# Optimization experiments

Measured on AMD Instinct MI355X. Metric: run time of the kernel, lower is better.

## Reference

```python
import jax, jax.numpy as jnp
import numpy as np

N_NODES = 100000
N_EDGES = 1600000
N_FEAT = 128
HIDDEN = 64
NUM_GRAPHS = 64


def setup_inputs() -> dict:
    key = jax.random.key(0)
    ks = jax.random.split(key, 10)
    x = jax.random.normal(ks[0], (N_NODES, N_FEAT), dtype=jnp.float32)
    W = jax.random.normal(ks[1], (N_FEAT, HIDDEN), dtype=jnp.float32) * (1.0 / np.sqrt(N_FEAT))
    b = jax.random.normal(ks[2], (HIDDEN,), dtype=jnp.float32) * 0.01
    W1 = jax.random.normal(ks[3], (HIDDEN, 16), dtype=jnp.float32) * (1.0 / np.sqrt(HIDDEN))
    b1 = jax.random.normal(ks[4], (16,), dtype=jnp.float32) * 0.01
    W2 = jax.random.normal(ks[5], (16, 1), dtype=jnp.float32) * 0.25
    b2 = jax.random.normal(ks[6], (1,), dtype=jnp.float32) * 0.01
    edge_index = jax.random.randint(ks[7], (2, N_EDGES), 0, N_NODES, dtype=jnp.int64)
    batch = jnp.sort(jax.random.randint(ks[8], (N_NODES,), 0, NUM_GRAPHS, dtype=jnp.int64))
    return {"x": x, "W": W, "b": b, "W1": W1, "b1": b1, "W2": W2, "b2": b2,
            "edge_index": edge_index, "batch": batch, "num_graphs": NUM_GRAPHS}


def reference(x, W, b, W1, b1, W2, b2, edge_index, batch, num_graphs):
    N = x.shape[0]
    # GCNConv: h = D^-1/2 (A + I) D^-1/2 (x W) + b
    h = x @ W  # [N, H]
    loops = jnp.arange(N, dtype=edge_index.dtype)
    src = jnp.concatenate([edge_index[0], loops])  # source nodes (with self-loops)
    dst = jnp.concatenate([edge_index[1], loops])  # target nodes
    deg = jax.ops.segment_sum(jnp.ones(dst.shape, h.dtype), dst, num_segments=N)
    dis = jnp.where(deg > 0, jax.lax.rsqrt(deg), 0.0)  # deg^-1/2, 0 for isolated
    norm = dis[src] * dis[dst]  # [E+N]
    msg = h[src] * norm[:, None]  # gather + normalize
    agg = jax.ops.segment_sum(msg, dst, num_segments=N) + b  # scatter-add + bias
    hn = jax.nn.relu(agg)
    # global_add_pool over graphs
    u = jax.ops.segment_sum(hn, batch, num_segments=num_graphs)  # [G, H]
    out = jax.nn.relu(u @ W1 + b1) @ W2 + b2  # [G, 1]
    return out.reshape(-1)
```

## Files before the change

kernel.cpp:

```cpp
#include <hip/hip_runtime.h>

#define N_NODES   100000
#define N_FEAT    128
#define N_EDGES   1600000
#define HIDDEN    64
#define NUM_GRAPHS 64
#define CHUNK   8192
#define NCHUNK  ((N_EDGES + CHUNK - 1) / CHUNK)
#define BSHIFT  8
#define NBUCKET ((N_NODES + 255) >> 8)
#define OFFS_W  (NBUCKET + 1)
#define CAP     4800
#define WT_BLOCKS 4
#define GEMM_GRID ((N_NODES + 127) / 128)

typedef unsigned int  uint32;
typedef unsigned short ushort16;

typedef __attribute__((ext_vector_type(8))) __bf16 bf16x8;
typedef __attribute__((ext_vector_type(4))) float  f32x4;
union Frag8 { bf16x8 v; unsigned short s[8]; uint4 q; };

static __device__ __forceinline__ unsigned short f2bf(float f) {
    uint32 u = __float_as_uint(f);
    u += 0x7fffu + ((u >> 16) & 1u);
    return (unsigned short)(u >> 16);
}

__global__ __launch_bounds__(512) void k_pre(const float* __restrict__ W,
                                             ushort16* __restrict__ Wt,
                                             const int* __restrict__ ei,
                                             int* __restrict__ src_out,
                                             unsigned char* __restrict__ dst8,
                                             int* __restrict__ offs) {
    __shared__ int hist[512];
    __shared__ int excl[512];
    __shared__ int ssrc[CHUNK];
    __shared__ int sdst[CHUNK];

    if (blockIdx.x < WT_BLOCKS) {
        const int base = blockIdx.x * 2048 + threadIdx.x;
#pragma unroll
        for (int j = 0; j < 4; ++j) {
            const int idx = base + j * 512;
            const int k = idx >> 6, n = idx & 63;
            Wt[n * N_FEAT + k] = f2bf(W[idx]);
        }
        return;
    }

    const int c = blockIdx.x - WT_BLOCKS;
    const int base = c * CHUNK;
    const int n = min(CHUNK, N_EDGES - base);
    const int t = threadIdx.x;
    hist[t] = 0;
    __syncthreads();

    int es[CHUNK / 512], ed[CHUNK / 512], rk[CHUNK / 512];
#pragma unroll
    for (int k = 0; k < CHUNK / 512; ++k) {
        const int i = t + k * 512;
        if (i < n) {
            ed[k] = __builtin_nontemporal_load(&ei[N_EDGES + base + i]);
            es[k] = __builtin_nontemporal_load(&ei[base + i]);
            rk[k] = atomicAdd(&hist[ed[k] >> BSHIFT], 1);
        }
    }
    __syncthreads();

    const int cnt = hist[t];
    for (int off = 1; off < 512; off <<= 1) {
        const int v = (t >= off) ? hist[t - off] : 0;
        __syncthreads();
        hist[t] += v;
        __syncthreads();
    }
    excl[t] = hist[t] - cnt;
    __syncthreads();
    if (t <= NBUCKET) offs[c * OFFS_W + t] = base + excl[t];

#pragma unroll
    for (int k = 0; k < CHUNK / 512; ++k) {
        const int i = t + k * 512;
        if (i < n) {
            const int pos = excl[ed[k] >> BSHIFT] + rk[k];
            ssrc[pos] = es[k];
            sdst[pos] = ed[k];
        }
    }
    __syncthreads();

    for (int i = t; i < n; i += 512)
        src_out[base + i] = ssrc[i];
    for (int i = t * 4; i < n; i += 2048) {
        const uint32 p = (uint32)(sdst[i] & 255)
                       | ((uint32)(sdst[i + 1] & 255) << 8)
                       | ((uint32)(sdst[i + 2] & 255) << 16)
                       | ((uint32)(sdst[i + 3] & 255) << 24);
        *(uint32*)&dst8[base + i] = p;
    }
}

__global__ __launch_bounds__(512) void k_mid(const float* __restrict__ x,
                                             const ushort16* __restrict__ Wt,
                                             ushort16* __restrict__ hb,
                                             const int* __restrict__ offs,
                                             const int* __restrict__ src_tmp,
                                             const unsigned char* __restrict__ dst8,
                                             int* __restrict__ srcs,
                                             int* __restrict__ row_ptr,
                                             int* __restrict__ row_end,
                                             float* __restrict__ dis) {
    __shared__ int hist[256];
    __shared__ int nxt[256];
    __shared__ int segb[NCHUNK];
    __shared__ int pre[NCHUNK + 1];
    __shared__ int sc[256];
    __shared__ int ssrc[CAP];
    __shared__ int sb;

    if (blockIdx.x >= NBUCKET) {
        const int t    = threadIdx.x;
        const int lane = t & 63;
        const int wv   = t >> 6;
        const int m15  = lane & 15;
        const int quad = lane >> 4;
        const int base = (blockIdx.x - NBUCKET) * 128 + wv * 16;
        const int arow = min(base + m15, N_NODES - 1);

        const float* xr = &x[(size_t)arow * N_FEAT + quad * 8];
        float4 xa[4][2];
#pragma unroll
        for (int kc = 0; kc < 4; ++kc) {
            xa[kc][0] = *(const float4*)&xr[kc * 32];
            xa[kc][1] = *(const float4*)&xr[kc * 32 + 4];
        }

        Frag8 bf[4][4];
#pragma unroll
        for (int nt = 0; nt < 4; ++nt) {
            const ushort16* wr = &Wt[(nt * 16 + m15) * N_FEAT + quad * 8];
#pragma unroll
            for (int kc = 0; kc < 4; ++kc)
                bf[nt][kc].q = *(const uint4*)&wr[kc * 32];
        }

        Frag8 af[4];
#pragma unroll
        for (int kc = 0; kc < 4; ++kc) {
            const float* f = (const float*)&xa[kc][0];
#pragma unroll
            for (int j = 0; j < 8; ++j) af[kc].s[j] = f2bf(f[j]);
        }

        f32x4 acc[4];
#pragma unroll
        for (int nt = 0; nt < 4; ++nt) acc[nt] = (f32x4){0.f, 0.f, 0.f, 0.f};

#pragma unroll
        for (int kc = 0; kc < 4; ++kc)
#pragma unroll
            for (int nt = 0; nt < 4; ++nt)
                acc[nt] = __builtin_amdgcn_mfma_f32_16x16x32_bf16(af[kc].v, bf[nt][kc].v,
                                                                  acc[nt], 0, 0, 0);

#pragma unroll
        for (int r = 0; r < 4; ++r) {
            const int orow = base + quad * 4 + r;
            if (orow < N_NODES) {
#pragma unroll
                for (int nt = 0; nt < 4; ++nt)
                    hb[(size_t)orow * HIDDEN + nt * 16 + m15] = f2bf(acc[nt][r]);
            }
        }
        return;
    }

    const int b = blockIdx.x;
    const int lo = b << BSHIFT;
    const int t = threadIdx.x;

    if (t < 256) hist[t] = 0;
    if (t == 0) sb = 0;
    __syncthreads();

    int len = 0;
    if (t < NCHUNK) {
        const int s0 = offs[t * OFFS_W + b];
        const int s1 = offs[t * OFFS_W + b + 1];
        segb[t] = s0;
        len = s1 - s0;
        atomicAdd(&sb, s0 - t * CHUNK);
    }
    if (t < 256) sc[t] = (t < NCHUNK) ? len : 0;
    __syncthreads();
    for (int off = 1; off < 256; off <<= 1) {
        int v = 0;
        if (t < 256 && t >= off) v = sc[t - off];
        __syncthreads();
        if (t < 256) sc[t] += v;
        __syncthreads();
    }
    if (t == 0) pre[0] = 0;
    if (t < NCHUNK) pre[t + 1] = sc[t];
    __syncthreads();

    const int total  = pre[NCHUNK];
    const int bstart = sb;
    const bool fits  = (total <= CAP);

    int es[(CAP + 511) / 512], ed[(CAP + 511) / 512], rk[(CAP + 511) / 512];
    int ne = 0;
    if (fits) {
        for (int e = t; e < total; e += 512) {
            int l2 = 0, h2 = NCHUNK;
            while (h2 - l2 > 1) { const int mid = (l2 + h2) >> 1;
                                  if (pre[mid] <= e) l2 = mid; else h2 = mid; }
            const int gidx = segb[l2] + (e - pre[l2]);
            const int d = dst8[gidx];
            const int s = src_tmp[gidx];
            es[ne] = s; ed[ne] = d;
            rk[ne] = atomicAdd(&hist[d], 1);
            ++ne;
        }
    } else {
        const int lane = t & 63, wv = t >> 6;
        for (int c = wv; c < NCHUNK; c += 8)
            for (int i = segb[c] + lane; i < segb[c] + (pre[c + 1] - pre[c]); i += 64)
                atomicAdd(&hist[dst8[i]], 1);
    }
    __syncthreads();

    const int cnt = (t < 256) ? hist[t] : 0;
    for (int off = 1; off < 256; off <<= 1) {
        int v = 0;
        if (t < 256 && t >= off) v = hist[t - off];
        __syncthreads();
        if (t < 256) hist[t] += v;
        __syncthreads();
    }
    if (t < 256) {
        const int excl = hist[t] - cnt;
        nxt[t] = excl;
        const int node = lo + t;
        if (node < N_NODES) {
            row_ptr[node] = bstart + excl;
            row_end[node] = bstart + excl + cnt;
            dis[node]     = rsqrtf((float)cnt + 1.0f);
        }
    }
    __syncthreads();

    if (fits) {
        for (int k = 0; k < ne; ++k)
            ssrc[nxt[ed[k]] + rk[k]] = es[k];
        __syncthreads();
        for (int i = t; i < total; i += 512)
            srcs[bstart + i] = ssrc[i];
    } else {
        const int lane = t & 63, wv = t >> 6;
        for (int c = wv; c < NCHUNK; c += 8)
            for (int i = segb[c] + lane; i < segb[c] + (pre[c + 1] - pre[c]); i += 64) {
                const int d = dst8[i];
                const int pos = atomicAdd(&nxt[d], 1);
                srcs[bstart + pos] = src_tmp[i];
            }
    }
}

__global__ __launch_bounds__(256) void agg_kernel(const int* __restrict__ row_ptr,
                                                  const int* __restrict__ row_end,
                                                  const int* __restrict__ srcs,
                                                  const ushort16* __restrict__ hb,
                                                  const float* __restrict__ dis,
                                                  const float* __restrict__ bias,
                                                  const int* __restrict__ batch,
                                                  float* __restrict__ u) {
    __shared__ float sp[32][HIDDEN + 1];
    __shared__ int gbs[32];
    const int t = threadIdx.x;
    const int lane = t & 63;
    const int wv = t >> 6;
    const int g = lane >> 3;
    const int k = lane & 7;
    const int kb = lane & 56;
    const int base = blockIdx.x * 32;
    const int node = base + wv * 8 + g;
    const int beg = row_ptr[node];
    const int end = row_end[node];
    const int deg = end - beg;
    const float dn = dis[node];

    int dmax = deg;
    dmax = max(dmax, __shfl_xor(dmax, 8));
    dmax = max(dmax, __shfl_xor(dmax, 16));
    dmax = max(dmax, __shfl_xor(dmax, 32));

    float acc[8];
#pragma unroll
    for (int j = 0; j < 8; ++j) acc[j] = 0.f;

    for (int i0 = 0; i0 < dmax; i0 += 8) {
        int idx = beg + i0 + k;
        idx = min(idx, end - 1);
        idx = max(idx, 0);
        const int s8 = srcs[idx];
        const float w8 = dis[s8] * dn;

        int   si[8];
        float wi[8];
#pragma unroll
        for (int j = 0; j < 8; ++j) {
            si[j] = __shfl(s8, kb | j);
            const float w = __shfl(w8, kb | j);
            wi[j] = (i0 + j < deg) ? w : 0.f;
        }
        uint4 v[8];
#pragma unroll
        for (int j = 0; j < 8; ++j)
            v[j] = *(const uint4*)&hb[(size_t)si[j] * HIDDEN + k * 8];
#pragma unroll
        for (int j = 0; j < 8; ++j) {
            acc[0] = fmaf(__uint_as_float(v[j].x << 16),         wi[j], acc[0]);
            acc[1] = fmaf(__uint_as_float(v[j].x & 0xffff0000u), wi[j], acc[1]);
            acc[2] = fmaf(__uint_as_float(v[j].y << 16),         wi[j], acc[2]);
            acc[3] = fmaf(__uint_as_float(v[j].y & 0xffff0000u), wi[j], acc[3]);
            acc[4] = fmaf(__uint_as_float(v[j].z << 16),         wi[j], acc[4]);
            acc[5] = fmaf(__uint_as_float(v[j].z & 0xffff0000u), wi[j], acc[5]);
            acc[6] = fmaf(__uint_as_float(v[j].w << 16),         wi[j], acc[6]);
            acc[7] = fmaf(__uint_as_float(v[j].w & 0xffff0000u), wi[j], acc[7]);
        }
    }

    {
        const uint4 hv = *(const uint4*)&hb[(size_t)node * HIDDEN + k * 8];
        const float d2 = dn * dn;
        const float4 b0 = *(const float4*)&bias[k * 8];
        const float4 b1 = *(const float4*)&bias[k * 8 + 4];
        float4 r0, r1;
        r0.x = fmaxf(fmaf(__uint_as_float(hv.x << 16),         d2, acc[0]) + b0.x, 0.f);
        r0.y = fmaxf(fmaf(__uint_as_float(hv.x & 0xffff0000u), d2, acc[1]) + b0.y, 0.f);
        r0.z = fmaxf(fmaf(__uint_as_float(hv.y << 16),         d2, acc[2]) + b0.z, 0.f);
        r0.w = fmaxf(fmaf(__uint_as_float(hv.y & 0xffff0000u), d2, acc[3]) + b0.w, 0.f);
        r1.x = fmaxf(fmaf(__uint_as_float(hv.z << 16),         d2, acc[4]) + b1.x, 0.f);
        r1.y = fmaxf(fmaf(__uint_as_float(hv.z & 0xffff0000u), d2, acc[5]) + b1.y, 0.f);
        r1.z = fmaxf(fmaf(__uint_as_float(hv.w << 16),         d2, acc[6]) + b1.z, 0.f);
        r1.w = fmaxf(fmaf(__uint_as_float(hv.w & 0xffff0000u), d2, acc[7]) + b1.w, 0.f);
        *(float4*)&sp[wv * 8 + g][k * 8]     = r0;
        *(float4*)&sp[wv * 8 + g][k * 8 + 4] = r1;
    }
    if (t < 32) gbs[t] = batch[base + t];
    __syncthreads();

    if (t < 64) {
        float a = sp[0][t];
        int cg = gbs[0];
        for (int r = 1; r < 32; ++r) {
            const int gr = gbs[r];
            const float vv = sp[r][t];
            if (gr == cg) a += vv;
            else { atomicAdd(&u[cg * HIDDEN + t], a); cg = gr; a = vv; }
        }
        atomicAdd(&u[cg * HIDDEN + t], a);
    }
}

__global__ __launch_bounds__(64) void mlp_kernel(const float* __restrict__ u,
                                                 const float* __restrict__ W1,
                                                 const float* __restrict__ b1,
                                                 const float* __restrict__ W2,
                                                 const float* __restrict__ b2,
                                                 float* __restrict__ out) {
    __shared__ float W1s[HIDDEN * 16];
    __shared__ float W2s[16];
    __shared__ float b1s[16];
    const int t = threadIdx.x;
    for (int i = t; i < HIDDEN * 16; i += 64) W1s[i] = W1[i];
    if (t < 16) { W2s[t] = W2[t]; b1s[t] = b1[t]; }
    __syncthreads();
    if (t < NUM_GRAPHS) {
        float uu[HIDDEN];
#pragma unroll
        for (int k = 0; k < HIDDEN; ++k) uu[k] = u[t * HIDDEN + k];
        float o = b2[0];
#pragma unroll
        for (int j = 0; j < 16; ++j) {
            float s = b1s[j];
#pragma unroll
            for (int k = 0; k < HIDDEN; ++k) s = fmaf(uu[k], W1s[k * 16 + j], s);
            o = fmaf(fmaxf(s, 0.f), W2s[j], o);
        }
        out[t] = o;
    }
}

extern "C" void kernel_launch(void* const* d_in, const int* in_sizes, int n_in,
                              void* d_out, int out_size, void* d_ws, size_t ws_size,
                              hipStream_t stream) {
    const float* x  = (const float*)d_in[0];
    const float* W  = (const float*)d_in[1];
    const float* b  = (const float*)d_in[2];
    const float* W1 = (const float*)d_in[3];
    const float* b1 = (const float*)d_in[4];
    const float* W2 = (const float*)d_in[5];
    const float* b2 = (const float*)d_in[6];
    const int*   ei = (const int*)d_in[7];
    const int* batch = (const int*)d_in[8];
    float* out = (float*)d_out;

    ushort16* hb       = (ushort16*)d_ws;
    int*      src_tmp  = (int*)(hb + (size_t)N_NODES * HIDDEN);
    unsigned char* dst8 = (unsigned char*)(src_tmp + N_EDGES);
    int*      srcs     = (int*)(dst8 + N_EDGES);
    int*      offs     = srcs + N_EDGES;
    int*      row_ptr  = offs + NCHUNK * OFFS_W;
    int*      row_end  = row_ptr + N_NODES;
    float*    dis      = (float*)(row_end + N_NODES);
    float*    u        = dis + N_NODES;
    ushort16* Wtg      = (ushort16*)(u + NUM_GRAPHS * HIDDEN);

    hipMemsetAsync(u, 0, NUM_GRAPHS * HIDDEN * sizeof(float), stream);

    k_pre<<<WT_BLOCKS + NCHUNK, 512, 0, stream>>>(W, Wtg, ei, src_tmp, dst8, offs);
    k_mid<<<NBUCKET + GEMM_GRID, 512, 0, stream>>>(x, Wtg, hb, offs, src_tmp, dst8,
                                                   srcs, row_ptr, row_end, dis);
    agg_kernel<<<N_NODES / 32, 256, 0, stream>>>(row_ptr, row_end, srcs, hb, dis, b, batch, u);
    mlp_kernel<<<1, 64, 0, stream>>>(u, W1, b1, W2, b2, out);
}
```

Measured before the change: 177.4 us.

## Prescale features by source degree norm and prefetch neighbor indices in aggregation

A new k_scale kernel multiplies each row of the bf16 hidden features by dis[node] once, so the aggregation loop no longer gathers dis[src] per edge and the destination normalization is applied once at the end. The aggregation loop now iterates per-node degree instead of the group maximum and software-prefetches the next batch of source indices. It also halves CHUNK (more chunks, a 512-wide scan) to give the bucketing pass more parallel blocks. The extra kernel adds a full read-write pass over hb and a second bf16 rounding of the scaled values, and per-lane divergent loop trip counts may add divergence.

Measured after the change: 175.4 us. No clear change (-1.1%).

```diff
diff --git a/kernel.cpp b/kernel.cpp
--- a/kernel.cpp
+++ b/kernel.cpp
@@ -5,7 +5,7 @@
 #define N_EDGES   1600000
 #define HIDDEN    64
 #define NUM_GRAPHS 64
-#define CHUNK   8192
+#define CHUNK   4096
 #define NCHUNK  ((N_EDGES + CHUNK - 1) / CHUNK)
 #define BSHIFT  8
 #define NBUCKET ((N_NODES + 255) >> 8)
@@ -115,7 +115,7 @@
     __shared__ int nxt[256];
     __shared__ int segb[NCHUNK];
     __shared__ int pre[NCHUNK + 1];
-    __shared__ int sc[256];
+    __shared__ int sc[512];
     __shared__ int ssrc[CAP];
     __shared__ int sb;
 
@@ -192,13 +192,12 @@
         len = s1 - s0;
         atomicAdd(&sb, s0 - t * CHUNK);
     }
-    if (t < 256) sc[t] = (t < NCHUNK) ? len : 0;
-    __syncthreads();
-    for (int off = 1; off < 256; off <<= 1) {
-        int v = 0;
-        if (t < 256 && t >= off) v = sc[t - off];
-        __syncthreads();
-        if (t < 256) sc[t] += v;
+    sc[t] = len;
+    __syncthreads();
+    for (int off = 1; off < 512; off <<= 1) {
+        const int v = (t >= off) ? sc[t - off] : 0;
+        __syncthreads();
+        sc[t] += v;
         __syncthreads();
     }
     if (t == 0) pre[0] = 0;
@@ -266,6 +265,23 @@
                 srcs[bstart + pos] = src_tmp[i];
             }
     }
+}
+
+__global__ __launch_bounds__(256) void k_scale(ushort16* __restrict__ hb,
+                                               const float* __restrict__ dis) {
+    const int i = blockIdx.x * 256 + threadIdx.x;
+    const float dn = dis[i >> 3];
+    uint4 v = *(const uint4*)&hb[(size_t)i * 8];
+    uint4 r;
+    r.x = (uint32)f2bf(__uint_as_float(v.x << 16) * dn)
+        | ((uint32)f2bf(__uint_as_float(v.x & 0xffff0000u) * dn) << 16);
+    r.y = (uint32)f2bf(__uint_as_float(v.y << 16) * dn)
+        | ((uint32)f2bf(__uint_as_float(v.y & 0xffff0000u) * dn) << 16);
+    r.z = (uint32)f2bf(__uint_as_float(v.z << 16) * dn)
+        | ((uint32)f2bf(__uint_as_float(v.z & 0xffff0000u) * dn) << 16);
+    r.w = (uint32)f2bf(__uint_as_float(v.w << 16) * dn)
+        | ((uint32)f2bf(__uint_as_float(v.w & 0xffff0000u) * dn) << 16);
+    *(uint4*)&hb[(size_t)i * 8] = r;
 }
 
 __global__ __launch_bounds__(256) void agg_kernel(const int* __restrict__ row_ptr,
@@ -291,61 +307,53 @@
     const int deg = end - beg;
     const float dn = dis[node];
 
-    int dmax = deg;
-    dmax = max(dmax, __shfl_xor(dmax, 8));
-    dmax = max(dmax, __shfl_xor(dmax, 16));
-    dmax = max(dmax, __shfl_xor(dmax, 32));
-
     float acc[8];
 #pragma unroll
     for (int j = 0; j < 8; ++j) acc[j] = 0.f;
 
-    for (int i0 = 0; i0 < dmax; i0 += 8) {
-        int idx = beg + i0 + k;
-        idx = min(idx, end - 1);
-        idx = max(idx, 0);
-        const int s8 = srcs[idx];
-        const float w8 = dis[s8] * dn;
-
-        int   si[8];
-        float wi[8];
-#pragma unroll
-        for (int j = 0; j < 8; ++j) {
-            si[j] = __shfl(s8, kb | j);
-            const float w = __shfl(w8, kb | j);
-            wi[j] = (i0 + j < deg) ? w : 0.f;
-        }
+    int pidx = max(min(beg + k, end - 1), 0);
+    int s8 = srcs[pidx];
+
+    for (int i0 = 0; i0 < deg; i0 += 8) {
+        const int rem = deg - i0;
+        const int cur = s8;
+        if (i0 + 8 < deg)
+            s8 = srcs[min(beg + i0 + 8 + k, end - 1)];
+
+        int si[8];
+#pragma unroll
+        for (int j = 0; j < 8; ++j) si[j] = __shfl(cur, kb | j);
         uint4 v[8];
 #pragma unroll
         for (int j = 0; j < 8; ++j)
             v[j] = *(const uint4*)&hb[(size_t)si[j] * HIDDEN + k * 8];
 #pragma unroll
         for (int j = 0; j < 8; ++j) {
-            acc[0] = fmaf(__uint_as_float(v[j].x << 16),         wi[j], acc[0]);
-            acc[1] = fmaf(__uint_as_float(v[j].x & 0xffff0000u), wi[j], acc[1]);
-            acc[2] = fmaf(__uint_as_float(v[j].y << 16),         wi[j], acc[2]);
-            acc[3] = fmaf(__uint_as_float(v[j].y & 0xffff0000u), wi[j], acc[3]);
-            acc[4] = fmaf(__uint_as_float(v[j].z << 16),         wi[j], acc[4]);
-            acc[5] = fmaf(__uint_as_float(v[j].z & 0xffff0000u), wi[j], acc[5]);
-            acc[6] = fmaf(__uint_as_float(v[j].w << 16),         wi[j], acc[6]);
-            acc[7] = fmaf(__uint_as_float(v[j].w & 0xffff0000u), wi[j], acc[7]);
+            const float m = (j < rem) ? 1.f : 0.f;
+            acc[0] = fmaf(__uint_as_float(v[j].x << 16),         m, acc[0]);
+            acc[1] = fmaf(__uint_as_float(v[j].x & 0xffff0000u), m, acc[1]);
+            acc[2] = fmaf(__uint_as_float(v[j].y << 16),         m, acc[2]);
+            acc[3] = fmaf(__uint_as_float(v[j].y & 0xffff0000u), m, acc[3]);
+            acc[4] = fmaf(__uint_as_float(v[j].z << 16),         m, acc[4]);
+            acc[5] = fmaf(__uint_as_float(v[j].z & 0xffff0000u), m, acc[5]);
+            acc[6] = fmaf(__uint_as_float(v[j].w << 16),         m, acc[6]);
+            acc[7] = fmaf(__uint_as_float(v[j].w & 0xffff0000u), m, acc[7]);
         }
     }
 
     {
         const uint4 hv = *(const uint4*)&hb[(size_t)node * HIDDEN + k * 8];
-        const float d2 = dn * dn;
         const float4 b0 = *(const float4*)&bias[k * 8];
         const float4 b1 = *(const float4*)&bias[k * 8 + 4];
         float4 r0, r1;
-        r0.x = fmaxf(fmaf(__uint_as_float(hv.x << 16),         d2, acc[0]) + b0.x, 0.f);
-        r0.y = fmaxf(fmaf(__uint_as_float(hv.x & 0xffff0000u), d2, acc[1]) + b0.y, 0.f);
-        r0.z = fmaxf(fmaf(__uint_as_float(hv.y << 16),         d2, acc[2]) + b0.z, 0.f);
-        r0.w = fmaxf(fmaf(__uint_as_float(hv.y & 0xffff0000u), d2, acc[3]) + b0.w, 0.f);
-        r1.x = fmaxf(fmaf(__uint_as_float(hv.z << 16),         d2, acc[4]) + b1.x, 0.f);
-        r1.y = fmaxf(fmaf(__uint_as_float(hv.z & 0xffff0000u), d2, acc[5]) + b1.y, 0.f);
-        r1.z = fmaxf(fmaf(__uint_as_float(hv.w << 16),         d2, acc[6]) + b1.z, 0.f);
-        r1.w = fmaxf(fmaf(__uint_as_float(hv.w & 0xffff0000u), d2, acc[7]) + b1.w, 0.f);
+        r0.x = fmaxf(fmaf(acc[0] + __uint_as_float(hv.x << 16),         dn, b0.x), 0.f);
+        r0.y = fmaxf(fmaf(acc[1] + __uint_as_float(hv.x & 0xffff0000u), dn, b0.y), 0.f);
+        r0.z = fmaxf(fmaf(acc[2] + __uint_as_float(hv.y << 16),         dn, b0.z), 0.f);
+        r0.w = fmaxf(fmaf(acc[3] + __uint_as_float(hv.y & 0xffff0000u), dn, b0.w), 0.f);
+        r1.x = fmaxf(fmaf(acc[4] + __uint_as_float(hv.z << 16),         dn, b1.x), 0.f);
+        r1.y = fmaxf(fmaf(acc[5] + __uint_as_float(hv.z & 0xffff0000u), dn, b1.y), 0.f);
+        r1.z = fmaxf(fmaf(acc[6] + __uint_as_float(hv.w << 16),         dn, b1.z), 0.f);
+        r1.w = fmaxf(fmaf(acc[7] + __uint_as_float(hv.w & 0xffff0000u), dn, b1.w), 0.f);
         *(float4*)&sp[wv * 8 + g][k * 8]     = r0;
         *(float4*)&sp[wv * 8 + g][k * 8 + 4] = r1;
     }
@@ -424,6 +432,7 @@
     k_pre<<<WT_BLOCKS + NCHUNK, 512, 0, stream>>>(W, Wtg, ei, src_tmp, dst8, offs);
     k_mid<<<NBUCKET + GEMM_GRID, 512, 0, stream>>>(x, Wtg, hb, offs, src_tmp, dst8,
                                                    srcs, row_ptr, row_end, dis);
+    k_scale<<<3125, 256, 0, stream>>>(hb, dis);
     agg_kernel<<<N_NODES / 32, 256, 0, stream>>>(row_ptr, row_end, srcs, hb, dis, b, batch, u);
     mlp_kernel<<<1, 64, 0, stream>>>(u, W1, b1, W2, b2, out);
 }
```
